# Optimization experiments

Measured on AMD Instinct MI355X. Metric: run time of the kernel, lower is better.

## Reference

```python
import jax, jax.numpy as jnp
import numpy as np

B, L, H = 4, 96, 512
R, T = 257, 21


def setup_inputs() -> dict:
    key = jax.random.key(0)
    ks = jax.random.split(key, 7)
    std_in = (2.0 / (H + 1 + R)) ** 0.5  # xavier_normal over [H+1, R]
    return {
        "layer1": jax.random.normal(ks[0], (B, L, H), jnp.float32),
        "layer2": jax.random.normal(ks[1], (B, L, H), jnp.float32),
        "layer3": jax.random.normal(ks[2], (B, L, H), jnp.float32),
        "W_1": jax.random.normal(ks[3], (H + 1, R), jnp.float32) * std_in,
        "W_2": jax.random.normal(ks[4], (H + 1, R), jnp.float32) * std_in,
        "W_3": jax.random.normal(ks[5], (H + 1, R), jnp.float32) * std_in,
        "W_l": jax.random.normal(ks[6], (1, R, T), jnp.float32),
    }


def reference(layer1, layer2, layer3, W_1, W_2, W_3, W_l):
    # Append bias-ones feature, as in the torch forward.
    ones = jnp.ones((*layer1.shape[:2], 1), layer1.dtype)
    l1 = jnp.concatenate([layer1, ones], axis=-1)  # [n, i, H+1]
    l2 = jnp.concatenate([layer2, ones], axis=-1)  # [n, j, H+1]
    l3 = jnp.concatenate([layer3, jnp.ones((*layer3.shape[:-1], 1), layer3.dtype)], axis=-1)
    # Factor the CP contraction: project each stream to rank space first.
    p1 = jnp.einsum("nia,ar->nir", l1, W_1)  # [n, i, r]
    p2 = jnp.einsum("njb,br->njr", l2, W_2)  # [n, j, r]
    p3 = jnp.einsum("nkc,cr->nkr", l3, W_3)  # [n, k, r]
    # Fold label map into one stream, then rank-reduce outer product.
    p3t = jnp.einsum("nkr,rt->ntkr", p3, W_l[0])  # [n, t, k, r]
    out = jnp.einsum("nir,njr,ntkr->ntijk", p1, p2, p3t)  # [n, t, i, j, k]
    return out
```

## Files before the change

### kernel.cpp

```cpp
#include <hip/hip_runtime.h>
#include <hip/hip_bf16.h>

#define RR 257
#define RP 288
#define TT 21

typedef __attribute__((ext_vector_type(4))) float f32x4;
typedef __attribute__((ext_vector_type(8))) short bf16x8;

union Pack8 { unsigned short s[8]; uint4 v; };

__device__ __forceinline__ unsigned short f2b(float f) {
    union { float f; unsigned u; } v; v.f = f;
    unsigned r = v.u + 0x7fffu + ((v.u >> 16) & 1u);
    return (unsigned short)(r >> 16);
}

__global__ __launch_bounds__(384) void proj_kernel(
    const float* __restrict__ l1, const float* __restrict__ l2, const float* __restrict__ l3,
    const float* __restrict__ W1, const float* __restrict__ W2, const float* __restrict__ W3,
    float* __restrict__ P1f, float* __restrict__ P2f, float* __restrict__ P3f)
{
    int bx = blockIdx.x;
    int grp = bx % 24;
    int n = (bx / 24) & 3;
    int s = bx / 96;
    const float* layer = (s == 0) ? l1 : (s == 1) ? l2 : l3;
    const float* W     = (s == 0) ? W1 : (s == 1) ? W2 : W3;
    int i0 = grp * 4;

    __shared__ __attribute__((aligned(16))) float x[2048];
    const float4* src = (const float4*)(layer + (n * 96 + i0) * 512);
    float4* xv = (float4*)x;
    for (int idx = threadIdx.x; idx < 512; idx += 384) xv[idx] = src[idx];
    __syncthreads();

    int r = threadIdx.x;
    if (r < RP) {
        float a0 = 0.f, a1 = 0.f, a2 = 0.f, a3 = 0.f;
        if (r < RR) {
            float b = W[512 * RR + r];
            a0 = a1 = a2 = a3 = b;
            #pragma unroll 8
            for (int a = 0; a < 512; ++a) {
                float wa = W[a * RR + r];
                a0 = fmaf(x[a], wa, a0);
                a1 = fmaf(x[512 + a], wa, a1);
                a2 = fmaf(x[1024 + a], wa, a2);
                a3 = fmaf(x[1536 + a], wa, a3);
            }
        }
        float* P = (s == 0) ? P1f : (s == 1) ? P2f : P3f;
        int base = (n * 96 + i0) * RP + r;
        P[base]          = a0;
        P[base + RP]     = a1;
        P[base + 2 * RP] = a2;
        P[base + 3 * RP] = a3;
    }
}

__global__ __launch_bounds__(256) void aprep_kernel(
    const float* __restrict__ P1f, const float* __restrict__ P2f,
    unsigned short* __restrict__ Af)
{
    int bx = blockIdx.x;
    int n = bx / 96, i = bx % 96;
    __shared__ __attribute__((aligned(16))) float p1row[RP];
    for (int r = threadIdx.x; r < RP; r += 256)
        p1row[r] = P1f[(n * 96 + i) * RP + r];
    __syncthreads();

    unsigned short* dst = Af + (size_t)(n * 576 + i * 6) * 9 * 512;
    for (int idx = threadIdx.x; idx < 3456; idx += 256) {
        int L = idx & 63;
        int rest = idx >> 6;
        int ks = rest % 9, rgl = rest / 9;
        int j = rgl * 16 + (L & 15);
        int k8 = ks * 32 + (L >> 4) * 8;
        const float* p2p = P2f + (n * 96 + j) * RP + k8;
        float4 b0 = *(const float4*)(p2p);
        float4 b1 = *(const float4*)(p2p + 4);
        float4 a0 = *(const float4*)(p1row + k8);
        float4 a1 = *(const float4*)(p1row + k8 + 4);
        Pack8 u;
        u.s[0] = f2b(a0.x * b0.x); u.s[1] = f2b(a0.y * b0.y);
        u.s[2] = f2b(a0.z * b0.z); u.s[3] = f2b(a0.w * b0.w);
        u.s[4] = f2b(a1.x * b1.x); u.s[5] = f2b(a1.y * b1.y);
        u.s[6] = f2b(a1.z * b1.z); u.s[7] = f2b(a1.w * b1.w);
        *(uint4*)(dst + (size_t)(rgl * 9 + ks) * 512 + L * 8) = u.v;
    }
}

__global__ __launch_bounds__(256) void bprep_kernel(
    const float* __restrict__ P3f, const float* __restrict__ Wl,
    unsigned short* __restrict__ Bf)
{
    int bx = blockIdx.x;
    int h = bx & 1;
    int t = (bx >> 1) % TT, n = bx / (2 * TT);
    __shared__ __attribute__((aligned(16))) float wl_lds[RP];
    for (int r = threadIdx.x; r < RP; r += 256)
        wl_lds[r] = (r < RR) ? Wl[r * TT + t] : 0.f;
    __syncthreads();

    unsigned short* dst = Bf + (size_t)(n * TT + t) * 6 * 9 * 512;
    for (int idx2 = threadIdx.x; idx2 < 1728; idx2 += 256) {
        int idx = h * 1728 + idx2;
        int L = idx & 63;
        int rest = idx >> 6;
        int ks = rest % 9, kg = rest / 9;
        int col = kg * 16 + (L & 15);
        int r8 = ks * 32 + (L >> 4) * 8;
        const float* p3p = P3f + (n * 96 + col) * RP + r8;
        float4 p0 = *(const float4*)(p3p);
        float4 p1 = *(const float4*)(p3p + 4);
        float4 w0 = *(const float4*)(wl_lds + r8);
        float4 w1 = *(const float4*)(wl_lds + r8 + 4);
        Pack8 u;
        u.s[0] = f2b(p0.x * w0.x); u.s[1] = f2b(p0.y * w0.y);
        u.s[2] = f2b(p0.z * w0.z); u.s[3] = f2b(p0.w * w0.w);
        u.s[4] = f2b(p1.x * w1.x); u.s[5] = f2b(p1.y * w1.y);
        u.s[6] = f2b(p1.z * w1.z); u.s[7] = f2b(p1.w * w1.w);
        *(uint4*)(dst + (size_t)(kg * 9 + ks) * 512 + L * 8) = u.v;
    }
}

#define LOADA(s, kss) { _Pragma("unroll") for (int mf = 0; mf < 6; ++mf) \
    fa[s][mf] = *(const bf16x8*)(abase + (mf * 9 + (kss)) * 512); }
#define LOADB(kss) { _Pragma("unroll") for (int nf = 0; nf < 6; ++nf) \
    fb[nf] = *(const bf16x8*)(lbase + (nf * 9 + (kss)) * 512); }
#define MFMAS(s) { _Pragma("unroll") for (int nf = 0; nf < 6; ++nf) { \
    _Pragma("unroll") for (int mf = 0; mf < 6; ++mf) \
      acc[mf][nf] = __builtin_amdgcn_mfma_f32_16x16x32_bf16(fb[nf], fa[s][mf], acc[mf][nf], 0, 0, 0); } }

__global__ __launch_bounds__(256, 2) void tri8_kernel(
    const unsigned short* __restrict__ Af, const unsigned short* __restrict__ Bf,
    float* __restrict__ out)
{
    int orig = blockIdx.x;
    int bx = (orig & 7) * 252 + (orig >> 3);
    int t = bx % TT;
    int mtn = bx / TT;
    int mt = mtn % 24;
    int n = mtn / 24;

    int tid = threadIdx.x, lane = tid & 63, wv = tid >> 6;

    __shared__ __attribute__((aligned(16))) unsigned short blds[27648];

    {
        const uint4* bsrc = (const uint4*)(Bf + (size_t)(n * TT + t) * 27648);
        uint4* bdst = (uint4*)blds;
        for (int idx = tid; idx < 3456; idx += 256) bdst[idx] = bsrc[idx];
    }
    __syncthreads();

    const unsigned short* abase =
        Af + (size_t)(n * 576 + mt * 24 + wv * 6) * 9 * 512 + lane * 8;
    const unsigned short* lbase = blds + lane * 8;

    f32x4 acc[6][6] = {};
    bf16x8 fa[2][6], fb[6];

    LOADA(0, 0);
    #pragma unroll
    for (int ks = 0; ks < 9; ++ks) {
        if (ks < 8) {
            if (ks & 1) { LOADA(0, ks + 1); } else { LOADA(1, ks + 1); }
        }
        LOADB(ks);
        if (ks & 1) { MFMAS(1); } else { MFMAS(0); }
    }

    __syncthreads();
    float* tb = (float*)blds + wv * 1600;
    int Llo = lane & 15, Lhi = lane >> 4;
    size_t outbase = ((size_t)(n * TT + t) * 9216 + mt * 384 + wv * 96) * 96;

    #pragma unroll
    for (int mf = 0; mf < 6; ++mf) {
        #pragma unroll
        for (int nf = 0; nf < 6; ++nf)
            *(f32x4*)&tb[Llo * 100 + nf * 16 + Lhi * 4] = acc[mf][nf];
        float* gdst = out + outbase + (size_t)mf * 16 * 96;
        #pragma unroll
        for (int q = 0; q < 6; ++q) {
            int fidx = q * 64 + lane;
            int ml = fidx / 24, k4 = fidx % 24;
            f32x4 vv = *(const f32x4*)&tb[ml * 100 + k4 * 4];
            __builtin_nontemporal_store(vv, (f32x4*)(gdst + (size_t)fidx * 4));
        }
    }
}

extern "C" void kernel_launch(void* const* d_in, const int* in_sizes, int n_in,
                              void* d_out, int out_size, void* d_ws, size_t ws_size,
                              hipStream_t stream) {
    const float* l1 = (const float*)d_in[0];
    const float* l2 = (const float*)d_in[1];
    const float* l3 = (const float*)d_in[2];
    const float* W1 = (const float*)d_in[3];
    const float* W2 = (const float*)d_in[4];
    const float* W3 = (const float*)d_in[5];
    const float* Wl = (const float*)d_in[6];

    float* P1f = (float*)d_ws;
    float* P2f = P1f + 384 * RP;
    float* P3f = P2f + 384 * RP;
    unsigned short* Af = (unsigned short*)(P3f + 384 * RP);
    unsigned short* Bf = Af + (size_t)4 * 576 * 9 * 512;

    proj_kernel<<<288, 384, 0, stream>>>(l1, l2, l3, W1, W2, W3, P1f, P2f, P3f);
    aprep_kernel<<<384, 256, 0, stream>>>(P1f, P2f, Af);
    bprep_kernel<<<168, 256, 0, stream>>>(P3f, Wl, Bf);
    tri8_kernel<<<2016, 256, 0, stream>>>(Af, Bf, (float*)d_out);
}
```

Measured before the change: 116.4 us.

## Split MFMA tile into three M passes interleaving compute with output stores

The triple-product GEMM kernel now processes each wave's 96 rows in three 32-row passes, each with its own accumulators, and writes results after each pass. A dedicated LDS staging buffer replaces reuse of the B tile region, so no block barrier is needed before the epilogue. The intent is to overlap global stores with subsequent MFMA work and lower register pressure. B fragments are re-read from LDS three times and LDS usage grows.

```diff
diff --git a/kernel.cpp b/kernel.cpp
--- a/kernel.cpp
+++ b/kernel.cpp
@@ -125,15 +125,15 @@
     }
 }
 
-#define LOADA(s, kss) { _Pragma("unroll") for (int mf = 0; mf < 6; ++mf) \
-    fa[s][mf] = *(const bf16x8*)(abase + (mf * 9 + (kss)) * 512); }
-#define LOADB(kss) { _Pragma("unroll") for (int nf = 0; nf < 6; ++nf) \
-    fb[nf] = *(const bf16x8*)(lbase + (nf * 9 + (kss)) * 512); }
+#define LDA(s, p, q2, kss) { _Pragma("unroll") for (int q = 0; q < 2; ++q) \
+    fa[s][q] = *(const bf16x8*)(abase + (((p) * 2 + q) * 9 + (kss)) * 512); (void)q2; }
+#define LDB(s, kss) { _Pragma("unroll") for (int nf = 0; nf < 6; ++nf) \
+    fb[s][nf] = *(const bf16x8*)(lbase + (nf * 9 + (kss)) * 512); }
 #define MFMAS(s) { _Pragma("unroll") for (int nf = 0; nf < 6; ++nf) { \
-    _Pragma("unroll") for (int mf = 0; mf < 6; ++mf) \
-      acc[mf][nf] = __builtin_amdgcn_mfma_f32_16x16x32_bf16(fb[nf], fa[s][mf], acc[mf][nf], 0, 0, 0); } }
-
-__global__ __launch_bounds__(256, 2) void tri8_kernel(
+    _Pragma("unroll") for (int q = 0; q < 2; ++q) \
+      acc[q][nf] = __builtin_amdgcn_mfma_f32_16x16x32_bf16(fb[s][nf], fa[s][q], acc[q][nf], 0, 0, 0); } }
+
+__global__ __launch_bounds__(256, 2) void tri10_kernel(
     const unsigned short* __restrict__ Af, const unsigned short* __restrict__ Bf,
     float* __restrict__ out)
 {
@@ -147,6 +147,7 @@
     int tid = threadIdx.x, lane = tid & 63, wv = tid >> 6;
 
     __shared__ __attribute__((aligned(16))) unsigned short blds[27648];
+    __shared__ __attribute__((aligned(16))) float tbuf[4][1600];
 
     {
         const uint4* bsrc = (const uint4*)(Bf + (size_t)(n * TT + t) * 27648);
@@ -159,36 +160,38 @@
         Af + (size_t)(n * 576 + mt * 24 + wv * 6) * 9 * 512 + lane * 8;
     const unsigned short* lbase = blds + lane * 8;
 
-    f32x4 acc[6][6] = {};
-    bf16x8 fa[2][6], fb[6];
-
-    LOADA(0, 0);
-    #pragma unroll
-    for (int ks = 0; ks < 9; ++ks) {
-        if (ks < 8) {
-            if (ks & 1) { LOADA(0, ks + 1); } else { LOADA(1, ks + 1); }
-        }
-        LOADB(ks);
-        if (ks & 1) { MFMAS(1); } else { MFMAS(0); }
-    }
-
-    __syncthreads();
-    float* tb = (float*)blds + wv * 1600;
+    float* tb = tbuf[wv];
     int Llo = lane & 15, Lhi = lane >> 4;
     size_t outbase = ((size_t)(n * TT + t) * 9216 + mt * 384 + wv * 96) * 96;
 
     #pragma unroll
-    for (int mf = 0; mf < 6; ++mf) {
+    for (int p = 0; p < 3; ++p) {
+        f32x4 acc[2][6] = {};
+        bf16x8 fa[2][2], fb[2][6];
+
+        LDA(0, p, 0, 0); LDB(0, 0);
         #pragma unroll
-        for (int nf = 0; nf < 6; ++nf)
-            *(f32x4*)&tb[Llo * 100 + nf * 16 + Lhi * 4] = acc[mf][nf];
-        float* gdst = out + outbase + (size_t)mf * 16 * 96;
+        for (int kp = 0; kp < 4; ++kp) {
+            LDA(1, p, 0, 2 * kp + 1); LDB(1, 2 * kp + 1);
+            MFMAS(0);
+            LDA(0, p, 0, 2 * kp + 2); LDB(0, 2 * kp + 2);
+            MFMAS(1);
+        }
+        MFMAS(0);
+
         #pragma unroll
-        for (int q = 0; q < 6; ++q) {
-            int fidx = q * 64 + lane;
-            int ml = fidx / 24, k4 = fidx % 24;
-            f32x4 vv = *(const f32x4*)&tb[ml * 100 + k4 * 4];
-            __builtin_nontemporal_store(vv, (f32x4*)(gdst + (size_t)fidx * 4));
+        for (int q2 = 0; q2 < 2; ++q2) {
+            #pragma unroll
+            for (int nf = 0; nf < 6; ++nf)
+                *(f32x4*)&tb[Llo * 100 + nf * 16 + Lhi * 4] = acc[q2][nf];
+            float* gdst = out + outbase + (size_t)(p * 32 + q2 * 16) * 96;
+            #pragma unroll
+            for (int q = 0; q < 6; ++q) {
+                int fidx = q * 64 + lane;
+                int ml = fidx / 24, k4 = fidx % 24;
+                f32x4 vv = *(const f32x4*)&tb[ml * 100 + k4 * 4];
+                __builtin_nontemporal_store(vv, (f32x4*)(gdst + (size_t)fidx * 4));
+            }
         }
     }
 }
@@ -213,5 +216,5 @@
     proj_kernel<<<288, 384, 0, stream>>>(l1, l2, l3, W1, W2, W3, P1f, P2f, P3f);
     aprep_kernel<<<384, 256, 0, stream>>>(P1f, P2f, Af);
     bprep_kernel<<<168, 256, 0, stream>>>(P3f, Wl, Bf);
-    tri8_kernel<<<2016, 256, 0, stream>>>(Af, Bf, (float*)d_out);
-}
+    tri10_kernel<<<2016, 256, 0, stream>>>(Af, Bf, (float*)d_out);
+}
```

Result: slower. 128.5 us (+10.5%).
